# Performance work log

Hardware: AMD Instinct MI355X
Metric: run time of the kernel (lower is better)

## Reference

```python
import jax, jax.numpy as jnp
import numpy as np

N = 100000      # nodes
E = 800000      # edges (avg degree 8)
D_IN = 128
D_OUT = 128
HOPS = 3        # K in SGConv


def setup_inputs() -> dict:
    key = jax.random.key(0)
    k1, k2, k3 = jax.random.split(key, 3)
    x = jax.random.normal(k1, (N, D_IN), dtype=jnp.float32)
    edge_index = jax.random.randint(k2, (2, E), 0, N, dtype=jnp.int64)
    # SGConv's final torch.nn.Linear(in_channels, out_channels)
    W = jax.random.normal(k3, (D_OUT, D_IN), dtype=jnp.float32) / np.sqrt(D_IN).astype(np.float32)
    b = jnp.zeros((D_OUT,), dtype=jnp.float32)
    return {"x": x, "edge_index": edge_index, "W": W, "b": b}


def reference(x, edge_index, W, b):
    n = x.shape[0]
    loop = jnp.arange(n, dtype=edge_index.dtype)
    # gcn_norm with add_self_loops=True (SGConv default)
    src = jnp.concatenate([edge_index[0], loop])  # message sources
    dst = jnp.concatenate([edge_index[1], loop])  # aggregation targets
    ones = jnp.ones(src.shape[0], dtype=x.dtype)
    deg = jax.ops.segment_sum(ones, dst, num_segments=n)
    dinv = jnp.where(deg > 0, jax.lax.rsqrt(deg), 0.0)
    norm = dinv[src] * dinv[dst]  # symmetric D^-1/2 A_hat D^-1/2 coefficients

    def hop(h, _):
        msg = h[src] * norm[:, None]                      # [E+N, D] gather
        return jax.ops.segment_sum(msg, dst, num_segments=n), None

    h, _ = jax.lax.scan(hop, x, None, length=HOPS)        # A_norm^K x
    return h @ W.T + b                                     # final linear
```

## Files before the change

kernel.cpp:

```cpp
#include <hip/hip_runtime.h>
#include <hip/hip_bf16.h>

#define DF 128


typedef __attribute__((ext_vector_type(8))) short shortx8;
typedef __attribute__((ext_vector_type(4))) float floatx4;

__device__ __forceinline__ unsigned short f32_to_bf16_rne(float f) {
    unsigned int u = __float_as_uint(f);
    unsigned int r = (u >> 16) & 1u;
    u += 0x7FFFu + r;
    return (unsigned short)(u >> 16);
}
__device__ __forceinline__ float bf16_lo(unsigned int w) { return __uint_as_float(w << 16); }
__device__ __forceinline__ float bf16_hi(unsigned int w) { return __uint_as_float(w & 0xffff0000u); }
__device__ __forceinline__ unsigned int pack_bf16(float x, float y) {
    return ((unsigned int)f32_to_bf16_rne(y) << 16) | (unsigned int)f32_to_bf16_rne(x);
}

__global__ void detect_flags_kernel(const unsigned int* __restrict__ ew, int enwords,
                                    const unsigned short* __restrict__ xh, int xnh,
                                    int* __restrict__ flagI, int* __restrict__ flagD) {
    __shared__ int eodd_nz;
    __shared__ int xbig;
    if (threadIdx.x == 0) { eodd_nz = 0; xbig = 0; }
    __syncthreads();
    int f1 = 0;
    for (int i = 1 + 2 * (int)threadIdx.x; i < enwords; i += 2 * (int)blockDim.x)
        if (ew[i] != 0u) f1 = 1;
    int c = 0;
    for (int i = 2 * (int)threadIdx.x; i < xnh; i += 2 * (int)blockDim.x) {
        unsigned int e = ((unsigned int)xh[i] >> 7) & 0xFFu;
        if (e >= 0xC0u) c++;
    }
    if (f1) eodd_nz = 1;
    if (c) atomicAdd(&xbig, c);
    __syncthreads();
    if (threadIdx.x == 0) {
        *flagI = (eodd_nz == 0) ? 1 : 0;
        *flagD = (xbig > 8) ? 0 : 1;
    }
}

__global__ __launch_bounds__(256) void count_deg_kernel(const int* __restrict__ eidx,
                                                        const int* __restrict__ flagI,
                                                        int E, int n, int* __restrict__ cnt) {
    int bucket = (int)(blockIdx.x & 7);
    int bsize = (n + 7) >> 3;
    int lo = bucket * bsize;
    int hi = lo + bsize; if (hi > n) hi = n;
    int nthr = (int)(gridDim.x >> 3) * (int)blockDim.x;
    int t0 = (int)(blockIdx.x >> 3) * (int)blockDim.x + (int)threadIdx.x;
    int isI64 = *flagI;
    const long long* p64 = (const long long*)eidx;
    for (int e = t0; e < E; e += nthr) {
        int d = isI64 ? (int)p64[(long long)E + e] : eidx[E + e];
        if (d < lo || d >= hi) continue;
        int s = isI64 ? (int)p64[e] : eidx[e];
        if (s < 0 || s >= n) continue;
        atomicAdd(&cnt[d], 1);
    }
}

__global__ void dinv_kernel(const int* __restrict__ cnt, float* __restrict__ dinv, int n) {
    int i = blockIdx.x * blockDim.x + threadIdx.x;
    if (i < n) dinv[i] = rsqrtf((float)(cnt[i] + 1));
}

__global__ void scan_blocks_kernel(const int* __restrict__ cnt, int* __restrict__ row_start,
                                   int* __restrict__ partials, int n) {
    __shared__ int s[256];
    int i = blockIdx.x * 256 + threadIdx.x;
    int v = (i < n) ? cnt[i] : 0;
    s[threadIdx.x] = v;
    __syncthreads();
    for (int off = 1; off < 256; off <<= 1) {
        int t = ((int)threadIdx.x >= off) ? s[threadIdx.x - off] : 0;
        __syncthreads();
        s[threadIdx.x] += t;
        __syncthreads();
    }
    if (i < n) row_start[i] = s[threadIdx.x] - v;
    if (threadIdx.x == 255) partials[blockIdx.x] = s[255];
}

__global__ void scan_partials_kernel(int* __restrict__ partials, int nparts) {
    __shared__ int s[512];
    int v = ((int)threadIdx.x < nparts) ? partials[threadIdx.x] : 0;
    s[threadIdx.x] = v;
    __syncthreads();
    for (int off = 1; off < 512; off <<= 1) {
        int t = ((int)threadIdx.x >= off) ? s[threadIdx.x - off] : 0;
        __syncthreads();
        s[threadIdx.x] += t;
        __syncthreads();
    }
    if ((int)threadIdx.x < nparts) partials[threadIdx.x] = s[threadIdx.x] - v;
}

__global__ void finalize_rows_kernel(int* __restrict__ row_start, const int* __restrict__ partials,
                                     const int* __restrict__ cnt, int* __restrict__ cursor, int n) {
    int i = blockIdx.x * 256 + threadIdx.x;
    if (i < n) {
        int r = row_start[i] + partials[blockIdx.x];
        row_start[i] = r;
        cursor[i] = r;
        if (i == n - 1) row_start[n] = r + cnt[i];
    }
}

__global__ __launch_bounds__(256) void scatter_kernel(const int* __restrict__ eidx,
                                                      const int* __restrict__ flagI,
                                                      int E, int n, const float* __restrict__ dinv,
                                                      int* __restrict__ cursor, int2* __restrict__ csr) {
    int bucket = (int)(blockIdx.x & 7);
    int bsize = (n + 7) >> 3;
    int lo = bucket * bsize;
    int hi = lo + bsize; if (hi > n) hi = n;
    int nthr = (int)(gridDim.x >> 3) * (int)blockDim.x;
    int t0 = (int)(blockIdx.x >> 3) * (int)blockDim.x + (int)threadIdx.x;
    int isI64 = *flagI;
    const long long* p64 = (const long long*)eidx;
    for (int e = t0; e < E; e += nthr) {
        int d = isI64 ? (int)p64[(long long)E + e] : eidx[E + e];
        if (d < lo || d >= hi) continue;
        int s = isI64 ? (int)p64[e] : eidx[e];
        if (s < 0 || s >= n) continue;
        int pos = atomicAdd(&cursor[d], 1);
        int2 pk;
        pk.x = s;
        pk.y = __float_as_int(dinv[s]);
        csr[pos] = pk;
    }
}

__global__ void cast_x_kernel(const void* __restrict__ x, uint2* __restrict__ xb,
                              const int* __restrict__ flagD, int nw2) {
    int i = blockIdx.x * blockDim.x + threadIdx.x;
    if (i >= nw2) return;
    if (*flagD) {
        xb[i] = ((const uint2*)x)[i];
    } else {
        float4 v = ((const float4*)x)[i];
        uint2 o;
        o.x = pack_bf16(v.x, v.y);
        o.y = pack_bf16(v.z, v.w);
        xb[i] = o;
    }
}

__global__ void cast_wb_kernel(const void* __restrict__ W, const void* __restrict__ b,
                               unsigned short* __restrict__ Wb, float* __restrict__ bias_f,
                               const int* __restrict__ flagD) {
    int i = blockIdx.x * 256 + threadIdx.x;
    int bf = *flagD;
    if (i < 128 * 128)
        Wb[i] = bf ? ((const unsigned short*)W)[i] : f32_to_bf16_rne(((const float*)W)[i]);
    if (i < 128)
        bias_f[i] = bf ? bf16_lo((unsigned int)((const unsigned short*)b)[i]) : ((const float*)b)[i];
}

__global__ __launch_bounds__(256) void hop_kernel(const uint4* __restrict__ hin,
                                                  uint4* __restrict__ hout,
                                                  const int2* __restrict__ csr,
                                                  const int* __restrict__ row_start,
                                                  const float* __restrict__ dinv, int n) {
    int gw = (int)((blockIdx.x * 256 + threadIdx.x) >> 6);
    int lane = (int)(threadIdx.x & 63);
    if (gw >= n) return;
    int e = lane >> 4, c = lane & 15;
    float di = dinv[gw];
    int beg = row_start[gw], end = row_start[gw + 1];
    uint4 sv = hin[(size_t)gw * 16 + c];
    float a0 = 0.f, a1 = 0.f, a2 = 0.f, a3 = 0.f, a4 = 0.f, a5 = 0.f, a6 = 0.f, a7 = 0.f;
    for (int j = beg + e; j < end; j += 4) {
        int2 ed = csr[j];
        float w = __int_as_float(ed.y);
        uint4 v = hin[(size_t)ed.x * 16 + c];
        a0 += w * bf16_lo(v.x); a1 += w * bf16_hi(v.x);
        a2 += w * bf16_lo(v.y); a3 += w * bf16_hi(v.y);
        a4 += w * bf16_lo(v.z); a5 += w * bf16_hi(v.z);
        a6 += w * bf16_lo(v.w); a7 += w * bf16_hi(v.w);
    }
    a0 += __shfl_xor(a0, 16); a0 += __shfl_xor(a0, 32);
    a1 += __shfl_xor(a1, 16); a1 += __shfl_xor(a1, 32);
    a2 += __shfl_xor(a2, 16); a2 += __shfl_xor(a2, 32);
    a3 += __shfl_xor(a3, 16); a3 += __shfl_xor(a3, 32);
    a4 += __shfl_xor(a4, 16); a4 += __shfl_xor(a4, 32);
    a5 += __shfl_xor(a5, 16); a5 += __shfl_xor(a5, 32);
    a6 += __shfl_xor(a6, 16); a6 += __shfl_xor(a6, 32);
    a7 += __shfl_xor(a7, 16); a7 += __shfl_xor(a7, 32);
    a0 = di * (a0 + di * bf16_lo(sv.x)); a1 = di * (a1 + di * bf16_hi(sv.x));
    a2 = di * (a2 + di * bf16_lo(sv.y)); a3 = di * (a3 + di * bf16_hi(sv.y));
    a4 = di * (a4 + di * bf16_lo(sv.z)); a5 = di * (a5 + di * bf16_hi(sv.z));
    a6 = di * (a6 + di * bf16_lo(sv.w)); a7 = di * (a7 + di * bf16_hi(sv.w));
    if (e == 0) {
        uint4 o;
        o.x = pack_bf16(a0, a1);
        o.y = pack_bf16(a2, a3);
        o.z = pack_bf16(a4, a5);
        o.w = pack_bf16(a6, a7);
        hout[(size_t)gw * 16 + c] = o;
    }
}

__global__ __launch_bounds__(256, 2) void linear_mfma_kernel(
        const unsigned short* __restrict__ h, const unsigned short* __restrict__ Wb,
        const float* __restrict__ bias_f, void* __restrict__ out,
        const int* __restrict__ flagD, int n) {
    int bf = *flagD;
    int wave = (int)(threadIdx.x >> 6);
    int lane = (int)(threadIdx.x & 63);
    int q = lane >> 4, m16 = lane & 15;

    shortx8 bfrag[8][4];
    float bias[8];
#pragma unroll
    for (int nt = 0; nt < 8; ++nt) {
        int wr = nt * 16 + m16;
#pragma unroll
        for (int t = 0; t < 4; ++t)
            bfrag[nt][t] = *(const shortx8*)&Wb[wr * 128 + t * 32 + q * 8];
        bias[nt] = bias_f[wr];
    }

    int nstrips = (n + 15) / 16;
    int wid = (int)blockIdx.x * 4 + wave;
    int nw = (int)gridDim.x * 4;
    for (int s = wid; s < nstrips; s += nw) {
        int row0 = s * 16;
        int arow = row0 + m16;
        if (arow >= n) arow = n - 1;
        shortx8 afrag[4];
#pragma unroll
        for (int t = 0; t < 4; ++t)
            afrag[t] = *(const shortx8*)&h[(size_t)arow * 128 + t * 32 + q * 8];

        floatx4 acc[8];
#pragma unroll
        for (int nt = 0; nt < 8; ++nt) acc[nt] = (floatx4){0.f, 0.f, 0.f, 0.f};
#pragma unroll
        for (int t = 0; t < 4; ++t)
#pragma unroll
            for (int nt = 0; nt < 8; ++nt)
                acc[nt] = __builtin_amdgcn_mfma_f32_16x16x32_bf16(afrag[t], bfrag[nt][t], acc[nt], 0, 0, 0);

#pragma unroll
        for (int nt = 0; nt < 8; ++nt)
#pragma unroll
            for (int r = 0; r < 4; ++r) {
                int row = row0 + q * 4 + r;
                if (row < n) {
                    float v = acc[nt][r] + bias[nt];
                    size_t oi = (size_t)row * 128 + nt * 16 + m16;
                    if (bf) ((unsigned short*)out)[oi] = f32_to_bf16_rne(v);
                    else    ((float*)out)[oi] = v;
                }
            }
    }
}

extern "C" void kernel_launch(void* const* d_in, const int* in_sizes, int n_in,
                              void* d_out, int out_size, void* d_ws, size_t ws_size,
                              hipStream_t stream) {
    const void* x = d_in[0];
    const int* eidx = (const int*)d_in[1];
    const void* W = d_in[2];
    const void* b = d_in[3];

    int n = in_sizes[0] / DF;
    int E = in_sizes[1] / 2;

    char* ws = (char*)d_ws;
    size_t off = 0;
    auto alloc = [&](size_t bytes) -> void* {
        void* p = ws + off;
        off = (off + bytes + 255) & ~(size_t)255;
        return p;
    };
    unsigned int* hb = (unsigned int*)alloc((size_t)n * 64 * 4);
    float* dinv      = (float*)alloc((size_t)n * 4);
    int*   cnt       = (int*)alloc((size_t)n * 4);
    int*   row_start = (int*)alloc((size_t)(n + 1) * 4);
    int*   cursor    = (int*)alloc((size_t)n * 4);
    int*   partials  = (int*)alloc(4096);
    int*   flagI     = (int*)alloc(256);
    int*   flagD     = (int*)alloc(256);
    unsigned short* Wb = (unsigned short*)alloc(128 * 128 * 2);
    float* bias_f    = (float*)alloc(128 * 4);
    int2*  csr       = (int2*)alloc((size_t)E * 8);
    unsigned int* xb = (unsigned int*)d_out;

    hipMemsetAsync(cnt, 0, (size_t)n * 4, stream);

    int enw = 8192; if (2 * E < enw) enw = 2 * E;
    int xnh = 16384; if (n * DF < xnh) xnh = n * DF;
    detect_flags_kernel<<<1, 256, 0, stream>>>((const unsigned int*)eidx, enw,
                                               (const unsigned short*)x, xnh, flagI, flagD);

    int nb = (n + 255) / 256;
    int ebgrid = 8 * 64;
    count_deg_kernel<<<ebgrid, 256, 0, stream>>>(eidx, flagI, E, n, cnt);
    dinv_kernel<<<nb, 256, 0, stream>>>(cnt, dinv, n);
    scan_blocks_kernel<<<nb, 256, 0, stream>>>(cnt, row_start, partials, n);
    scan_partials_kernel<<<1, 512, 0, stream>>>(partials, nb);
    finalize_rows_kernel<<<nb, 256, 0, stream>>>(row_start, partials, cnt, cursor, n);
    scatter_kernel<<<ebgrid, 256, 0, stream>>>(eidx, flagI, E, n, dinv, cursor, csr);

    int nw2 = n * 32;
    cast_x_kernel<<<(nw2 + 255) / 256, 256, 0, stream>>>(x, (uint2*)xb, flagD, nw2);
    cast_wb_kernel<<<64, 256, 0, stream>>>(W, b, Wb, bias_f, flagD);

    int hb_grid = (n + 3) / 4;
    hop_kernel<<<hb_grid, 256, 0, stream>>>((const uint4*)xb, (uint4*)hb, csr, row_start, dinv, n);
    hop_kernel<<<hb_grid, 256, 0, stream>>>((const uint4*)hb, (uint4*)xb, csr, row_start, dinv, n);
    hop_kernel<<<hb_grid, 256, 0, stream>>>((const uint4*)xb, (uint4*)hb, csr, row_start, dinv, n);

    int nstrips = (n + 15) / 16;
    int lgrid = 512; if ((nstrips + 3) / 4 < lgrid) lgrid = (nstrips + 3) / 4;
    linear_mfma_kernel<<<lgrid, 256, 0, stream>>>(
        (const unsigned short*)hb, Wb, bias_f, d_out, flagD, n);
}
```

Measured before the change: 386.1 us.

## Build CSR with atomic rank capture instead of second cursor atomic pass

The degree-count kernel now records the return value of each atomicAdd as the edge's rank within its destination row. The scatter kernel then computes each position as row_start plus rank, with no atomics and no cursor array. The 8-bucket multi-pass edge scan in both kernels is replaced by a single flat pass with four edges per thread, and dinv is folded into finalize_rows, dropping one launch. The cost is an extra E-sized rank buffer that is written and read back, and atomics now hit random destinations across all nodes instead of one bucket at a time.

```diff
diff --git a/kernel.cpp b/kernel.cpp
--- a/kernel.cpp
+++ b/kernel.cpp
@@ -43,29 +43,37 @@
     }
 }
 
-__global__ __launch_bounds__(256) void count_deg_kernel(const int* __restrict__ eidx,
-                                                        const int* __restrict__ flagI,
-                                                        int E, int n, int* __restrict__ cnt) {
-    int bucket = (int)(blockIdx.x & 7);
-    int bsize = (n + 7) >> 3;
-    int lo = bucket * bsize;
-    int hi = lo + bsize; if (hi > n) hi = n;
-    int nthr = (int)(gridDim.x >> 3) * (int)blockDim.x;
-    int t0 = (int)(blockIdx.x >> 3) * (int)blockDim.x + (int)threadIdx.x;
+__global__ __launch_bounds__(256) void count_rank_kernel(const int* __restrict__ eidx,
+                                                         const int* __restrict__ flagI,
+                                                         int E, int n, int* __restrict__ cnt,
+                                                         int* __restrict__ rank) {
+    int t = blockIdx.x * blockDim.x + threadIdx.x;
+    int base = t * 4;
+    if (base >= E) return;
     int isI64 = *flagI;
     const long long* p64 = (const long long*)eidx;
-    for (int e = t0; e < E; e += nthr) {
-        int d = isI64 ? (int)p64[(long long)E + e] : eidx[E + e];
-        if (d < lo || d >= hi) continue;
-        int s = isI64 ? (int)p64[e] : eidx[e];
-        if (s < 0 || s >= n) continue;
-        atomicAdd(&cnt[d], 1);
-    }
-}
-
-__global__ void dinv_kernel(const int* __restrict__ cnt, float* __restrict__ dinv, int n) {
-    int i = blockIdx.x * blockDim.x + threadIdx.x;
-    if (i < n) dinv[i] = rsqrtf((float)(cnt[i] + 1));
+    int s[4], d[4];
+#pragma unroll
+    for (int j = 0; j < 4; ++j) {
+        int e = base + j;
+        if (e < E) {
+            if (isI64) { s[j] = (int)p64[e]; d[j] = (int)p64[(long long)E + e]; }
+            else       { s[j] = eidx[e];     d[j] = eidx[E + e]; }
+        } else { s[j] = -1; d[j] = -1; }
+    }
+    int r[4];
+#pragma unroll
+    for (int j = 0; j < 4; ++j) {
+        bool ok = ((unsigned)d[j] < (unsigned)n) && ((unsigned)s[j] < (unsigned)n);
+        r[j] = ok ? atomicAdd(&cnt[d[j]], 1) : 0;
+    }
+    if (base + 3 < E) {
+        *(int4*)&rank[base] = make_int4(r[0], r[1], r[2], r[3]);
+    } else {
+#pragma unroll
+        for (int j = 0; j < 4; ++j)
+            if (base + j < E) rank[base + j] = r[j];
+    }
 }
 
 __global__ void scan_blocks_kernel(const int* __restrict__ cnt, int* __restrict__ row_start,
@@ -100,38 +108,58 @@
 }
 
 __global__ void finalize_rows_kernel(int* __restrict__ row_start, const int* __restrict__ partials,
-                                     const int* __restrict__ cnt, int* __restrict__ cursor, int n) {
+                                     const int* __restrict__ cnt, float* __restrict__ dinv, int n) {
     int i = blockIdx.x * 256 + threadIdx.x;
     if (i < n) {
         int r = row_start[i] + partials[blockIdx.x];
         row_start[i] = r;
-        cursor[i] = r;
+        dinv[i] = rsqrtf((float)(cnt[i] + 1));
         if (i == n - 1) row_start[n] = r + cnt[i];
     }
 }
 
 __global__ __launch_bounds__(256) void scatter_kernel(const int* __restrict__ eidx,
                                                       const int* __restrict__ flagI,
+                                                      const int* __restrict__ rank,
+                                                      const int* __restrict__ row_start,
                                                       int E, int n, const float* __restrict__ dinv,
-                                                      int* __restrict__ cursor, int2* __restrict__ csr) {
-    int bucket = (int)(blockIdx.x & 7);
-    int bsize = (n + 7) >> 3;
-    int lo = bucket * bsize;
-    int hi = lo + bsize; if (hi > n) hi = n;
-    int nthr = (int)(gridDim.x >> 3) * (int)blockDim.x;
-    int t0 = (int)(blockIdx.x >> 3) * (int)blockDim.x + (int)threadIdx.x;
+                                                      int2* __restrict__ csr) {
+    int t = blockIdx.x * blockDim.x + threadIdx.x;
+    int base = t * 4;
+    if (base >= E) return;
     int isI64 = *flagI;
     const long long* p64 = (const long long*)eidx;
-    for (int e = t0; e < E; e += nthr) {
-        int d = isI64 ? (int)p64[(long long)E + e] : eidx[E + e];
-        if (d < lo || d >= hi) continue;
-        int s = isI64 ? (int)p64[e] : eidx[e];
-        if (s < 0 || s >= n) continue;
-        int pos = atomicAdd(&cursor[d], 1);
-        int2 pk;
-        pk.x = s;
-        pk.y = __float_as_int(dinv[s]);
-        csr[pos] = pk;
+    int s[4], d[4], r[4];
+    if (base + 3 < E) {
+        int4 rv = *(const int4*)&rank[base];
+        r[0] = rv.x; r[1] = rv.y; r[2] = rv.z; r[3] = rv.w;
+#pragma unroll
+        for (int j = 0; j < 4; ++j) {
+            int e = base + j;
+            if (isI64) { s[j] = (int)p64[e]; d[j] = (int)p64[(long long)E + e]; }
+            else       { s[j] = eidx[e];     d[j] = eidx[E + e]; }
+        }
+    } else {
+#pragma unroll
+        for (int j = 0; j < 4; ++j) {
+            int e = base + j;
+            if (e < E) {
+                r[j] = rank[e];
+                if (isI64) { s[j] = (int)p64[e]; d[j] = (int)p64[(long long)E + e]; }
+                else       { s[j] = eidx[e];     d[j] = eidx[E + e]; }
+            } else { s[j] = -1; d[j] = -1; r[j] = 0; }
+        }
+    }
+#pragma unroll
+    for (int j = 0; j < 4; ++j) {
+        bool ok = ((unsigned)d[j] < (unsigned)n) && ((unsigned)s[j] < (unsigned)n);
+        if (ok) {
+            int pos = row_start[d[j]] + r[j];
+            int2 pk;
+            pk.x = s[j];
+            pk.y = __float_as_int(dinv[s[j]]);
+            csr[pos] = pk;
+        }
     }
 }
 
@@ -283,13 +311,13 @@
     float* dinv      = (float*)alloc((size_t)n * 4);
     int*   cnt       = (int*)alloc((size_t)n * 4);
     int*   row_start = (int*)alloc((size_t)(n + 1) * 4);
-    int*   cursor    = (int*)alloc((size_t)n * 4);
     int*   partials  = (int*)alloc(4096);
     int*   flagI     = (int*)alloc(256);
     int*   flagD     = (int*)alloc(256);
     unsigned short* Wb = (unsigned short*)alloc(128 * 128 * 2);
     float* bias_f    = (float*)alloc(128 * 4);
     int2*  csr       = (int2*)alloc((size_t)E * 8);
+    int*   rank      = (int*)alloc((size_t)E * 4);
     unsigned int* xb = (unsigned int*)d_out;
 
     hipMemsetAsync(cnt, 0, (size_t)n * 4, stream);
@@ -300,13 +328,13 @@
                                                (const unsigned short*)x, xnh, flagI, flagD);
 
     int nb = (n + 255) / 256;
-    int ebgrid = 8 * 64;
-    count_deg_kernel<<<ebgrid, 256, 0, stream>>>(eidx, flagI, E, n, cnt);
-    dinv_kernel<<<nb, 256, 0, stream>>>(cnt, dinv, n);
+    int e4 = (E + 3) / 4;
+    int ebgrid = (e4 + 255) / 256;
+    count_rank_kernel<<<ebgrid, 256, 0, stream>>>(eidx, flagI, E, n, cnt, rank);
     scan_blocks_kernel<<<nb, 256, 0, stream>>>(cnt, row_start, partials, n);
     scan_partials_kernel<<<1, 512, 0, stream>>>(partials, nb);
-    finalize_rows_kernel<<<nb, 256, 0, stream>>>(row_start, partials, cnt, cursor, n);
-    scatter_kernel<<<ebgrid, 256, 0, stream>>>(eidx, flagI, E, n, dinv, cursor, csr);
+    finalize_rows_kernel<<<nb, 256, 0, stream>>>(row_start, partials, cnt, dinv, n);
+    scatter_kernel<<<ebgrid, 256, 0, stream>>>(eidx, flagI, rank, row_start, E, n, dinv, csr);
 
     int nw2 = n * 32;
     cast_x_kernel<<<(nw2 + 255) / 256, 256, 0, stream>>>(x, (uint2*)xb, flagD, nw2);
```

After: 330.5 us. 1.17x faster.
